# Kernel tuning notes

Hardware: AMD Instinct MI355X
Metric: run time of the kernel (lower is better)

Reference implementation:

```python
import jax, jax.numpy as jnp
import numpy as np
from jax.scipy.linalg import expm

NUM_QUBITS = 10
D = 2 ** NUM_QUBITS  # 1024
B, S = 8, 4096


def setup_inputs() -> dict:
    key = jax.random.key(0)
    k_x, k_mr, k_mi = jax.random.split(key, 3)
    inputs = jax.random.normal(k_x, (B, S, D), dtype=jnp.float32)
    M_real = 0.1 * jax.random.normal(k_mr, (D, D), dtype=jnp.float32)
    M_imag = 0.1 * jax.random.normal(k_mi, (D, D), dtype=jnp.float32)
    bias = jnp.zeros((D,), dtype=jnp.float32)
    qubit_gate = jnp.ones((D,), dtype=jnp.float32)
    return {"inputs": inputs, "M_real": M_real, "M_imag": M_imag,
            "bias": bias, "qubit_gate": qubit_gate}


def _l2_normalize(x, axis=-1, eps=1e-12):
    # matches tf.linalg.l2_normalize: x * rsqrt(max(sum(x^2), eps))
    ss = jnp.sum(jnp.square(x), axis=axis, keepdims=True)
    return x * jax.lax.rsqrt(jnp.maximum(ss, eps))


def reference(inputs, M_real, M_imag, bias, qubit_gate):
    norm_inputs = _l2_normalize(inputs, axis=-1)
    A = M_real - M_real.T  # skew-symmetric -> expm(A) is orthogonal
    Bm = M_imag - M_imag.T
    U = expm(A) @ expm(Bm)  # [D, D]
    transformed = jnp.einsum('bsd,de->bse', norm_inputs, U) + bias
    measured = jnp.square(transformed)
    gate_probs = jax.nn.softmax(qubit_gate)  # [D]
    gated_output = measured * gate_probs
    return gated_output, gate_probs
```

## Files before the change

### kernel.cpp

```cpp
#include <hip/hip_runtime.h>


typedef unsigned int u32;
typedef unsigned short u16;
typedef __attribute__((ext_vector_type(8))) short short8;
typedef __attribute__((ext_vector_type(4))) float f32x4;

#define GLOBAL_AS __attribute__((address_space(1)))
#define LDS_AS    __attribute__((address_space(3)))

constexpr int D = 1024;
constexpr float EXPM_SCALE = 1.0f / 8.0f;

__device__ __forceinline__ u16 f2bf(float f) {
  union { float f; u32 u; } v; v.f = f;
  u32 r = (v.u + 0x7FFFu + ((v.u >> 16) & 1u)) >> 16;
  return (u16)r;
}
__device__ __forceinline__ float bf2f(u16 u) {
  union { u32 u; float f; } v; v.u = ((u32)u) << 16;
  return v.f;
}

__device__ __forceinline__ void g2l16(const void* g, void* l) {
  __builtin_amdgcn_global_load_lds((const GLOBAL_AS u32*)g, (LDS_AS u32*)l,
                                   16, 0, 0);
}

#define WAITV(N)                                                   \
  do {                                                             \
    asm volatile("s_waitcnt vmcnt(" #N ")" ::: "memory");          \
    __builtin_amdgcn_sched_barrier(0);                             \
  } while (0)

__device__ void norm_rows8(const float* __restrict__ x, u16* __restrict__ Xn,
                           int r0, int tid, float* sred) {
  float4 v[8];
#pragma unroll
  for (int i = 0; i < 8; ++i)
    v[i] = ((const float4*)(x + (size_t)(r0 + i) * D))[tid];
  float ss[8];
#pragma unroll
  for (int i = 0; i < 8; ++i)
    ss[i] = v[i].x * v[i].x + v[i].y * v[i].y + v[i].z * v[i].z +
            v[i].w * v[i].w;
  for (int o = 32; o; o >>= 1)
#pragma unroll
    for (int i = 0; i < 8; ++i) ss[i] += __shfl_down(ss[i], o);
  const int w = tid >> 6;
  if ((tid & 63) == 0)
#pragma unroll
    for (int i = 0; i < 8; ++i) sred[i * 4 + w] = ss[i];
  __syncthreads();
#pragma unroll
  for (int i = 0; i < 8; ++i) {
    const float tot =
        sred[i * 4 + 0] + sred[i * 4 + 1] + sred[i * 4 + 2] + sred[i * 4 + 3];
    const float inv = rsqrtf(fmaxf(tot, 1e-12f));
    ushort4 o4;
    o4.x = f2bf(v[i].x * inv); o4.y = f2bf(v[i].y * inv);
    o4.z = f2bf(v[i].z * inv); o4.w = f2bf(v[i].w * inv);
    ((ushort4*)(Xn + (size_t)(r0 + i) * D))[tid] = o4;
  }
}

struct SkewParams {
  const float *Mr, *Mi;
  u16 *X0, *X1;
  const float* x;
  u16* Xn;
  int row0;
};
__global__ __launch_bounds__(256) void skew_norm_kernel(SkewParams p) {
  __shared__ __align__(16) float t2[64][67];
  const int bid = blockIdx.x, tid = threadIdx.x;
  if (bid >= 512) {
    norm_rows8(p.x, p.Xn, p.row0 + (bid - 512) * 8, tid, &t2[0][0]);
    return;
  }
  const int z = bid >> 8, t = bid & 255;
  const float* M = z ? p.Mi : p.Mr;
  u16* X = z ? p.X1 : p.X0;
  const int bi = t >> 4, bj = t & 15;
  const int r0 = tid >> 4, c0 = (tid & 15) * 4;
  float4 own[4];
#pragma unroll
  for (int i = 0; i < 4; ++i) {
    const int r = i * 16 + r0;
    own[i] = *(const float4*)(M + (size_t)(bi * 64 + r) * D + bj * 64 + c0);
    const float4 tr =
        *(const float4*)(M + (size_t)(bj * 64 + r) * D + bi * 64 + c0);
    t2[r][c0 + 0] = tr.x; t2[r][c0 + 1] = tr.y;
    t2[r][c0 + 2] = tr.z; t2[r][c0 + 3] = tr.w;
  }
  __syncthreads();
#pragma unroll
  for (int i = 0; i < 4; ++i) {
    const int r = i * 16 + r0;
    const float o[4] = {own[i].x, own[i].y, own[i].z, own[i].w};
    ushort4 hv;
    u16* hp = (u16*)&hv;
#pragma unroll
    for (int j = 0; j < 4; ++j)
      hp[j] = f2bf((o[j] - t2[c0 + j][r]) * EXPM_SCALE);
    *(ushort4*)(X + (size_t)(bi * 64 + r) * D + bj * 64 + c0) = hv;
  }
}

struct CJob {
  const u16 *A, *B;
  const float* C;
  u16 *Dst, *DT;
  float alpha;
};
struct GNParams {
  CJob jobs[2];
  int njobs;
  const float* x;
  u16* Xn;
  int row0;
};
__global__ __launch_bounds__(256) void gemm_norm_kernel(GNParams p) {
  __shared__ __align__(16) u16 ldsA[2][64 * 64];
  __shared__ __align__(16) u16 ldsB[2][64 * 64];
  const int bid = blockIdx.x, tid = threadIdx.x;
  if (bid >= p.njobs) {
    norm_rows8(p.x, p.Xn, p.row0 + (bid - p.njobs) * 8, tid,
               (float*)&ldsA[0][0]);
    return;
  }
  const CJob jb = p.jobs[bid >> 8];
  const int bi = (bid >> 4) & 15, bj = bid & 15;
  const int w = tid >> 6, lane = tid & 63;
  const int wr = w >> 1, wc = w & 1;
  f32x4 acc[2][2];
#pragma unroll
  for (int m = 0; m < 2; ++m)
#pragma unroll
    for (int n = 0; n < 2; ++n) acc[m][n] = f32x4{0.f, 0.f, 0.f, 0.f};
  const int r_l = lane >> 3, c_l = lane & 7;

  auto stage = [&](int buf, int kt) {
    const int k0 = kt * 64;
#pragma unroll
    for (int pp = 0; pp < 2; ++pp) {
      const int row = pp * 32 + w * 8 + r_l;
      const int chunk = c_l ^ (row & 7);
      g2l16(jb.A + (size_t)(bi * 64 + row) * D + k0 + chunk * 8,
            (char*)&ldsA[buf][0] + pp * 4096 + w * 1024);
      g2l16(jb.B + (size_t)(bj * 64 + row) * D + k0 + chunk * 8,
            (char*)&ldsB[buf][0] + pp * 4096 + w * 1024);
    }
  };

  stage(0, 0);
  __syncthreads();
  int buf = 0;
  for (int kt = 0; kt < 16; ++kt) {
    if (kt < 15) stage(buf ^ 1, kt + 1);
#pragma unroll
    for (int h = 0; h < 2; ++h) {
      const int kk = h * 32 + (lane >> 4) * 8;
      short8 a[2], b[2];
#pragma unroll
      for (int m = 0; m < 2; ++m) {
        const int row = wr * 32 + m * 16 + (lane & 15);
        const int off = row * 128 + ((kk * 2) ^ ((row & 7) << 4));
        a[m] = *(const short8*)((const char*)&ldsA[buf][0] + off);
      }
#pragma unroll
      for (int n = 0; n < 2; ++n) {
        const int row = wc * 32 + n * 16 + (lane & 15);
        const int off = row * 128 + ((kk * 2) ^ ((row & 7) << 4));
        b[n] = *(const short8*)((const char*)&ldsB[buf][0] + off);
      }
#pragma unroll
      for (int m = 0; m < 2; ++m)
#pragma unroll
        for (int n = 0; n < 2; ++n)
          acc[m][n] = __builtin_amdgcn_mfma_f32_16x16x32_bf16(
              a[m], b[n], acc[m][n], 0, 0, 0);
    }
    __syncthreads();
    buf ^= 1;
  }
  const int or0 = bi * 64 + wr * 32, oc0 = bj * 64 + wc * 32;
#pragma unroll
  for (int m = 0; m < 2; ++m)
#pragma unroll
    for (int n = 0; n < 2; ++n) {
      const int row0 = or0 + m * 16 + (lane >> 4) * 4;
      const int col = oc0 + n * 16 + (lane & 15);
      ushort4 dv;
      u16* dp = (u16*)&dv;
#pragma unroll
      for (int r = 0; r < 4; ++r) {
        float v = acc[m][n][r] * jb.alpha;
        if (jb.C) v += jb.C[(size_t)(row0 + r) * D + col];
        dp[r] = f2bf(v);
        jb.Dst[(size_t)(row0 + r) * D + col] = dp[r];
      }
      if (jb.DT)
        *(ushort4*)(jb.DT + (size_t)col * D + row0) = dv;
    }
}

struct X34Params {
  const u16 *X[2], *X2[2];
  u16 *X3[2], *X4[2], *q1t[2];
  float* q0[2];
  const float* qg;
  float* gate_out;
  const float* x;
  u16* Xn;
  int row0;
};
__global__ __launch_bounds__(256) void x34q_norm_kernel(X34Params p) {
  __shared__ __align__(16) u16 ldsA[2][64 * 64];
  __shared__ __align__(16) u16 ldsB1[2][64 * 64];
  __shared__ __align__(16) u16 ldsB2[2][64 * 64];
  const int bid = blockIdx.x, tid = threadIdx.x;
  if (bid > 512) {
    norm_rows8(p.x, p.Xn, p.row0 + (bid - 513) * 8, tid, (float*)&ldsA[0][0]);
    return;
  }
  if (bid == 512) {
    float* red = (float*)&ldsA[0][0];
    const float4 v = ((const float4*)p.qg)[tid];
    float mx = fmaxf(fmaxf(v.x, v.y), fmaxf(v.z, v.w));
    for (int o = 32; o; o >>= 1) mx = fmaxf(mx, __shfl_xor(mx, o));
    if ((tid & 63) == 0) red[tid >> 6] = mx;
    __syncthreads();
    const float M = fmaxf(fmaxf(red[0], red[1]), fmaxf(red[2], red[3]));
    __syncthreads();
    const float e0 = __expf(v.x - M), e1 = __expf(v.y - M),
                e2 = __expf(v.z - M), e3 = __expf(v.w - M);
    float s = e0 + e1 + e2 + e3;
    for (int o = 32; o; o >>= 1) s += __shfl_xor(s, o);
    if ((tid & 63) == 0) red[tid >> 6] = s;
    __syncthreads();
    const float S = red[0] + red[1] + red[2] + red[3];
    const float4 o4 = {e0 / S, e1 / S, e2 / S, e3 / S};
    ((float4*)p.gate_out)[tid] = o4;
    return;
  }
  const int mz = bid >> 8, t = bid & 255;
  const int bi = t >> 4, bj = t & 15;
  const u16* Ag = p.X2[mz];
  const u16* B1g = p.X[mz];
  const u16* B2g = p.X2[mz];
  const int w = tid >> 6, lane = tid & 63;
  const int wr = w >> 1, wc = w & 1;
  f32x4 acc3[2][2], acc4[2][2];
#pragma unroll
  for (int m = 0; m < 2; ++m)
#pragma unroll
    for (int n = 0; n < 2; ++n) {
      acc3[m][n] = f32x4{0.f, 0.f, 0.f, 0.f};
      acc4[m][n] = f32x4{0.f, 0.f, 0.f, 0.f};
    }
  const int r_l = lane >> 3, c_l = lane & 7;

  auto stage = [&](int buf, int kt) {
    const int k0 = kt * 64;
#pragma unroll
    for (int pp = 0; pp < 2; ++pp) {
      const int row = pp * 32 + w * 8 + r_l;
      const int chunk = c_l ^ (row & 7);
      g2l16(Ag + (size_t)(bi * 64 + row) * D + k0 + chunk * 8,
            (char*)&ldsA[buf][0] + pp * 4096 + w * 1024);
      g2l16(B1g + (size_t)(bj * 64 + row) * D + k0 + chunk * 8,
            (char*)&ldsB1[buf][0] + pp * 4096 + w * 1024);
      g2l16(B2g + (size_t)(bj * 64 + row) * D + k0 + chunk * 8,
            (char*)&ldsB2[buf][0] + pp * 4096 + w * 1024);
    }
  };

  stage(0, 0);
  __syncthreads();
  int buf = 0;
  for (int kt = 0; kt < 16; ++kt) {
    if (kt < 15) stage(buf ^ 1, kt + 1);
#pragma unroll
    for (int h = 0; h < 2; ++h) {
      const int kk = h * 32 + (lane >> 4) * 8;
      short8 a[2], b1[2], b2[2];
#pragma unroll
      for (int m = 0; m < 2; ++m) {
        const int row = wr * 32 + m * 16 + (lane & 15);
        const int off = row * 128 + ((kk * 2) ^ ((row & 7) << 4));
        a[m] = *(const short8*)((const char*)&ldsA[buf][0] + off);
      }
#pragma unroll
      for (int n = 0; n < 2; ++n) {
        const int row = wc * 32 + n * 16 + (lane & 15);
        const int off = row * 128 + ((kk * 2) ^ ((row & 7) << 4));
        b1[n] = *(const short8*)((const char*)&ldsB1[buf][0] + off);
        b2[n] = *(const short8*)((const char*)&ldsB2[buf][0] + off);
      }
#pragma unroll
      for (int m = 0; m < 2; ++m)
#pragma unroll
        for (int n = 0; n < 2; ++n) {
          acc3[m][n] = __builtin_amdgcn_mfma_f32_16x16x32_bf16(
              a[m], b1[n], acc3[m][n], 0, 0, 0);
          acc4[m][n] = __builtin_amdgcn_mfma_f32_16x16x32_bf16(
              a[m], b2[n], acc4[m][n], 0, 0, 0);
        }
    }
    __syncthreads();
    buf ^= 1;
  }
  const int or0 = bi * 64 + wr * 32, oc0 = bj * 64 + wc * 32;
#pragma unroll
  for (int m = 0; m < 2; ++m)
#pragma unroll
    for (int n = 0; n < 2; ++n) {
      const int row0 = or0 + m * 16 + (lane >> 4) * 4;
      const int col = oc0 + n * 16 + (lane & 15);
#pragma unroll
      for (int r = 0; r < 4; ++r) {
        const size_t idx = (size_t)(row0 + r) * D + col;
        const u16 x3v = f2bf(-acc3[m][n][r]);
        const u16 x4v = f2bf(acc4[m][n][r]);
        p.X3[mz][idx] = x3v;
        p.X4[mz][idx] = x4v;
        const float d = (row0 + r == col) ? 1.f : 0.f;
        const float xf = bf2f(p.X[mz][idx]);
        const float x2f = bf2f(p.X2[mz][idx]);
        const float x3f = bf2f(x3v), x4f = bf2f(x4v);
        p.q0[mz][idx] = d + xf + x2f * 0.5f + x3f * (1.f / 6.f);
        p.q1t[mz][idx] =
            f2bf(d * (1.f / 24.f) - xf * (1.f / 120.f) + x2f * (1.f / 720.f) -
                 x3f * (1.f / 5040.f) + x4f * (1.f / 40320.f));
      }
    }
}

__global__ __launch_bounds__(512, 1) void main_gemm_kernel(
    const u16* __restrict__ Xn, const u16* __restrict__ Wm,
    const float* __restrict__ bias, const float* __restrict__ gate,
    float* __restrict__ out) {
  const int tid = threadIdx.x;
  const int wid = tid >> 6, lane = tid & 63;
  const int wr = wid >> 2, wc = wid & 3;
  __shared__ u16 lds[4 * 16384];
  f32x4 acc[8][4];
#pragma unroll
  for (int m = 0; m < 8; ++m)
#pragma unroll
    for (int n = 0; n < 4; ++n) acc[m][n] = f32x4{0.f, 0.f, 0.f, 0.f};

  const int bi = blockIdx.x, bj = blockIdx.y;
  const int r_ = tid >> 2;
  const int c_ = tid & 3;

  auto stage = [&](int s) {
    char* base = (char*)lds + (s & 3) * 32768;
#pragma unroll
    for (int pp = 0; pp < 2; ++pp) {
      const int row = pp * 128 + r_;
      const int csrc = c_ ^ ((row >> 1) & 3);
      g2l16(Xn + (size_t)(bi * 256 + row) * D + s * 32 + csrc * 8,
            base + pp * 8192 + tid * 16);
      g2l16(Wm + (size_t)(bj * 256 + row) * D + s * 32 + csrc * 8,
            base + 16384 + pp * 8192 + tid * 16);
    }
  };

  const int h = lane >> 4;
  auto compute = [&](int s) {
    const char* base = (const char*)lds + (s & 3) * 32768;
    short8 a[8], b[4];
#pragma unroll
    for (int m = 0; m < 8; ++m) {
      const int row = wr * 128 + m * 16 + (lane & 15);
      const int off = row * 64 + ((h ^ ((row >> 1) & 3)) << 4);
      a[m] = *(const short8*)(base + off);
    }
#pragma unroll
    for (int n = 0; n < 4; ++n) {
      const int row = wc * 64 + n * 16 + (lane & 15);
      const int off = 16384 + row * 64 + ((h ^ ((row >> 1) & 3)) << 4);
      b[n] = *(const short8*)(base + off);
    }
    __builtin_amdgcn_s_setprio(1);
#pragma unroll
    for (int m = 0; m < 8; ++m)
#pragma unroll
      for (int n = 0; n < 4; ++n)
        acc[m][n] = __builtin_amdgcn_mfma_f32_16x16x32_bf16(a[m], b[n],
                                                            acc[m][n], 0, 0, 0);
    __builtin_amdgcn_s_setprio(0);
  };

  stage(0); stage(1); stage(2);
  for (int s = 0; s < 29; ++s) {
    WAITV(8);
    __builtin_amdgcn_s_barrier();
    __builtin_amdgcn_sched_barrier(0);
    stage(s + 3);
    compute(s);
  }
  WAITV(8);
  __builtin_amdgcn_s_barrier();
  __builtin_amdgcn_sched_barrier(0);
  compute(29);
  WAITV(4);
  __builtin_amdgcn_s_barrier();
  __builtin_amdgcn_sched_barrier(0);
  compute(30);
  WAITV(0);
  __builtin_amdgcn_s_barrier();
  __builtin_amdgcn_sched_barrier(0);
  compute(31);

  const int or0 = bi * 256 + wr * 128, oc0 = bj * 256 + wc * 64;
#pragma unroll
  for (int m = 0; m < 8; ++m)
#pragma unroll
    for (int n = 0; n < 4; ++n) {
      const int col = oc0 + n * 16 + (lane & 15);
      const float bc = bias[col], gc = gate[col];
#pragma unroll
      for (int r = 0; r < 4; ++r) {
        const int row = or0 + m * 16 + (lane >> 4) * 4 + r;
        const float t = acc[m][n][r] + bc;
        out[(size_t)row * D + col] = t * t * gc;
      }
    }
}

extern "C" void kernel_launch(void* const* d_in, const int* in_sizes, int n_in,
                              void* d_out, int out_size, void* d_ws,
                              size_t ws_size, hipStream_t stream) {
  (void)in_sizes; (void)n_in; (void)out_size; (void)ws_size;
  const float* inp = (const float*)d_in[0];
  const float* Mr = (const float*)d_in[1];
  const float* Mi = (const float*)d_in[2];
  const float* bias = (const float*)d_in[3];
  const float* qg = (const float*)d_in[4];
  float* out = (float*)d_out;
  float* gate_out = out + (size_t)32768 * 1024;

  char* ws = (char*)d_ws;
  u16* Xn = (u16*)ws;
  auto slot = [&](int m, int s) -> u16* {
    return (u16*)(ws + 67108864 + (size_t)m * 16777216 + (size_t)s * 2097152);
  };
  auto q0p = [&](int m) -> float* {
    return (float*)(ws + 67108864 + (size_t)m * 16777216 + 12582912);
  };
  u16* W = (u16*)(ws + 100663296);

  const int CH = 4096, NB = 512;
  int row0 = 0;

  {
    SkewParams sp{Mr, Mi, slot(0, 0), slot(1, 0), inp, Xn, row0};
    skew_norm_kernel<<<512 + NB, 256, 0, stream>>>(sp);
    row0 += CH;
  }
  GNParams gp{};
  gp.x = inp; gp.Xn = Xn;
  for (int m = 0; m < 2; ++m)
    gp.jobs[m] = CJob{slot(m, 0), slot(m, 0), nullptr, slot(m, 1), nullptr,
                      -1.f};
  gp.njobs = 512; gp.row0 = row0;
  gemm_norm_kernel<<<512 + NB, 256, 0, stream>>>(gp);
  row0 += CH;
  {
    X34Params xp{};
    for (int m = 0; m < 2; ++m) {
      xp.X[m] = slot(m, 0); xp.X2[m] = slot(m, 1);
      xp.X3[m] = slot(m, 2); xp.X4[m] = slot(m, 3);
      xp.q1t[m] = slot(m, 4); xp.q0[m] = q0p(m);
    }
    xp.qg = qg; xp.gate_out = gate_out;
    xp.x = inp; xp.Xn = Xn; xp.row0 = row0;
    x34q_norm_kernel<<<513 + NB, 256, 0, stream>>>(xp);
    row0 += CH;
  }
  for (int m = 0; m < 2; ++m)
    gp.jobs[m] = CJob{slot(m, 3), slot(m, 4), q0p(m), slot(m, 0), slot(m, 1),
                      1.f};
  gp.njobs = 512; gp.row0 = row0;
  gemm_norm_kernel<<<512 + NB, 256, 0, stream>>>(gp);
  row0 += CH;
  for (int m = 0; m < 2; ++m)
    gp.jobs[m] = CJob{slot(m, 0), slot(m, 1), nullptr, slot(m, 2), slot(m, 4),
                      1.f};
  gp.row0 = row0;
  gemm_norm_kernel<<<512 + NB, 256, 0, stream>>>(gp);
  row0 += CH;
  for (int m = 0; m < 2; ++m)
    gp.jobs[m] = CJob{slot(m, 2), slot(m, 4), nullptr, slot(m, 3), slot(m, 5),
                      1.f};
  gp.row0 = row0;
  gemm_norm_kernel<<<512 + NB, 256, 0, stream>>>(gp);
  row0 += CH;
  for (int m = 0; m < 2; ++m)
    gp.jobs[m] = CJob{slot(m, 3), slot(m, 5), nullptr, slot(m, 0), slot(m, 1),
                      1.f};
  gp.row0 = row0;
  gemm_norm_kernel<<<512 + NB, 256, 0, stream>>>(gp);
  row0 += CH;
  gp.jobs[0] = CJob{slot(1, 1), slot(0, 0), nullptr, W, nullptr, 1.f};
  gp.njobs = 256; gp.row0 = row0;
  gemm_norm_kernel<<<256 + NB, 256, 0, stream>>>(gp);

  main_gemm_kernel<<<dim3(128, 4), 512, 0, stream>>>(Xn, W, bias, gate_out,
                                                     out);
}
```

Before: 236.0 us.

## Deepen LDS pipelining in expm GEMM kernels with multi-stage buffers and vmcnt waits

Replaces the double-buffered K loop in the two expm-stage GEMM kernels with a 4-stage (gemm_norm) and 3-stage (x34q) ring of LDS buffers. Each step waits on a partial vmcnt count and issues a single barrier instead of a full __syncthreads, so several global-to-LDS loads stay in flight while MFMA runs. The goal is to hide global load latency in these small 1024x1024 GEMMs. In exchange it uses more LDS per block, which may lower occupancy, and relies on WAITV counts matching the number of loads issued per stage.

```diff
diff --git a/kernel.cpp b/kernel.cpp
--- a/kernel.cpp
+++ b/kernel.cpp
@@ -121,8 +121,8 @@
   int row0;
 };
 __global__ __launch_bounds__(256) void gemm_norm_kernel(GNParams p) {
-  __shared__ __align__(16) u16 ldsA[2][64 * 64];
-  __shared__ __align__(16) u16 ldsB[2][64 * 64];
+  __shared__ __align__(16) u16 ldsA[4][4096];
+  __shared__ __align__(16) u16 ldsB[4][4096];
   const int bid = blockIdx.x, tid = threadIdx.x;
   if (bid >= p.njobs) {
     norm_rows8(p.x, p.Xn, p.row0 + (bid - p.njobs) * 8, tid,
@@ -152,12 +152,8 @@
             (char*)&ldsB[buf][0] + pp * 4096 + w * 1024);
     }
   };
-
-  stage(0, 0);
-  __syncthreads();
-  int buf = 0;
-  for (int kt = 0; kt < 16; ++kt) {
-    if (kt < 15) stage(buf ^ 1, kt + 1);
+  auto compute = [&](int buf, int kt) {
+    (void)kt;
 #pragma unroll
     for (int h = 0; h < 2; ++h) {
       const int kk = h * 32 + (lane >> 4) * 8;
@@ -181,9 +177,29 @@
           acc[m][n] = __builtin_amdgcn_mfma_f32_16x16x32_bf16(
               a[m], b[n], acc[m][n], 0, 0, 0);
     }
-    __syncthreads();
-    buf ^= 1;
-  }
+  };
+
+  stage(0, 0); stage(1, 1); stage(2, 2);
+  for (int s = 0; s < 13; ++s) {
+    WAITV(8);
+    __builtin_amdgcn_s_barrier();
+    __builtin_amdgcn_sched_barrier(0);
+    stage((s + 3) & 3, s + 3);
+    compute(s & 3, s);
+  }
+  WAITV(8);
+  __builtin_amdgcn_s_barrier();
+  __builtin_amdgcn_sched_barrier(0);
+  compute(13 & 3, 13);
+  WAITV(4);
+  __builtin_amdgcn_s_barrier();
+  __builtin_amdgcn_sched_barrier(0);
+  compute(14 & 3, 14);
+  WAITV(0);
+  __builtin_amdgcn_s_barrier();
+  __builtin_amdgcn_sched_barrier(0);
+  compute(15 & 3, 15);
+
   const int or0 = bi * 64 + wr * 32, oc0 = bj * 64 + wc * 32;
 #pragma unroll
   for (int m = 0; m < 2; ++m)
@@ -216,9 +232,9 @@
   int row0;
 };
 __global__ __launch_bounds__(256) void x34q_norm_kernel(X34Params p) {
-  __shared__ __align__(16) u16 ldsA[2][64 * 64];
-  __shared__ __align__(16) u16 ldsB1[2][64 * 64];
-  __shared__ __align__(16) u16 ldsB2[2][64 * 64];
+  __shared__ __align__(16) u16 ldsA[3][4096];
+  __shared__ __align__(16) u16 ldsB1[3][4096];
+  __shared__ __align__(16) u16 ldsB2[3][4096];
   const int bid = blockIdx.x, tid = threadIdx.x;
   if (bid > 512) {
     norm_rows8(p.x, p.Xn, p.row0 + (bid - 513) * 8, tid, (float*)&ldsA[0][0]);
@@ -275,12 +291,8 @@
             (char*)&ldsB2[buf][0] + pp * 4096 + w * 1024);
     }
   };
-
-  stage(0, 0);
-  __syncthreads();
-  int buf = 0;
-  for (int kt = 0; kt < 16; ++kt) {
-    if (kt < 15) stage(buf ^ 1, kt + 1);
+  auto compute = [&](int buf, int kt) {
+    (void)kt;
 #pragma unroll
     for (int h = 0; h < 2; ++h) {
       const int kk = h * 32 + (lane >> 4) * 8;
@@ -308,9 +320,27 @@
               a[m], b2[n], acc4[m][n], 0, 0, 0);
         }
     }
-    __syncthreads();
-    buf ^= 1;
-  }
+  };
+
+  stage(0, 0); stage(1, 1);
+  int c0 = 0, c1 = 1, c2 = 2;
+  for (int s = 0; s < 14; ++s) {
+    WAITV(6);
+    __builtin_amdgcn_s_barrier();
+    __builtin_amdgcn_sched_barrier(0);
+    stage(c2, s + 2);
+    compute(c0, s);
+    const int tswap = c0; c0 = c1; c1 = c2; c2 = tswap;
+  }
+  WAITV(6);
+  __builtin_amdgcn_s_barrier();
+  __builtin_amdgcn_sched_barrier(0);
+  compute(c0, 14);
+  WAITV(0);
+  __builtin_amdgcn_s_barrier();
+  __builtin_amdgcn_sched_barrier(0);
+  compute(c1, 15);
+
   const int or0 = bi * 64 + wr * 32, oc0 = bj * 64 + wc * 32;
 #pragma unroll
   for (int m = 0; m < 2; ++m)
```

Result: faster. 229.0 us (-3.0%).
